# Performance work log

Hardware: AMD Instinct MI355X
Metric: run time of the kernel (lower is better)

Reference implementation:

```python
import jax, jax.numpy as jnp
import numpy as np

UP = 4  # FCUUp up_stride
EPS_FCU = 1e-6
EPS_NL = 1e-5


def setup_inputs() -> dict:
    key = jax.random.key(0)
    ks = jax.random.split(key, 24)
    B, E, C, CI = 8, 768, 256, 128
    H, W = 14, 14
    x_t = jax.random.normal(ks[0], (B, 1 + H * W, E), jnp.float32)
    x_cnn = jax.random.normal(ks[1], (B, C, H * UP, W * UP), jnp.float32)
    s = 0.02
    return {
        'x_t': x_t,
        'x_cnn': x_cnn,
        # FCUUp: conv_project (E->C) + BN
        'Wp': jax.random.normal(ks[2], (C, E), jnp.float32) * s,
        'bp': jnp.zeros((C,), jnp.float32),
        'g1': jnp.ones((C,), jnp.float32),
        'b1': jnp.zeros((C,), jnp.float32),
        'rm1': jax.random.normal(ks[3], (C,), jnp.float32) * 0.1,
        'rv1': jax.random.uniform(ks[4], (C,), jnp.float32, 0.5, 1.5),
        # NLBlockND (embedded): g, theta, phi 1x1 convs C->CI
        'Wg': jax.random.normal(ks[5], (CI, C), jnp.float32) * s,
        'bg': jnp.zeros((CI,), jnp.float32),
        'Wth': jax.random.normal(ks[6], (CI, C), jnp.float32) * s,
        'bth': jnp.zeros((CI,), jnp.float32),
        'Wph': jax.random.normal(ks[7], (CI, C), jnp.float32) * s,
        'bph': jnp.zeros((CI,), jnp.float32),
        # W_z: 1x1 conv CI->C + BN
        'Wz': jax.random.normal(ks[8], (C, CI), jnp.float32) * s,
        'bz': jnp.zeros((C,), jnp.float32),
        'g2': jax.random.normal(ks[9], (C,), jnp.float32) * 0.1,
        'b2': jax.random.normal(ks[10], (C,), jnp.float32) * 0.1,
        'rm2': jax.random.normal(ks[11], (C,), jnp.float32) * 0.1,
        'rv2': jax.random.uniform(ks[12], (C,), jnp.float32, 0.5, 1.5),
    }


def _bn(x, gamma, beta, mean, var, eps):
    # eval-mode BatchNorm2d over channel axis 1 of BCHW
    inv = gamma / jnp.sqrt(var + eps)
    return x * inv[None, :, None, None] + (beta - mean * inv)[None, :, None, None]


def _conv1x1(x, w, b):
    # x: BCHW, w: [O, C] -> BOHW
    return jnp.einsum('oc,bchw->bohw', w, x) + b[None, :, None, None]


def reference(x_t, x_cnn, Wp, bp, g1, b1, rm1, rv1, Wg, bg, Wth, bth, Wph, bph, Wz, bz, g2, b2, rm2, rv2):
    B, Nc, H2, W2 = x_cnn.shape
    H, W = H2 // UP, W2 // UP
    CI = Wg.shape[0]
    # --- FCUUp: tokens -> feature map ---
    xr = x_t[:, 1:].transpose(0, 2, 1).reshape(B, -1, H, W)  # B,E,H,W
    xr = jax.nn.relu(_bn(_conv1x1(xr, Wp, bp), g1, b1, rm1, rv1, EPS_FCU))
    x_up = jnp.repeat(jnp.repeat(xr, UP, axis=2), UP, axis=3)  # nearest interp -> B,C,H2,W2
    # --- NLBlockND embedded: this=x_cnn, other=x_up ---
    N = H2 * W2
    g_x = _conv1x1(x_cnn, Wg, bg).reshape(B, CI, N).transpose(0, 2, 1)   # B,N,CI
    theta = _conv1x1(x_cnn, Wth, bth).reshape(B, CI, N)                  # B,CI,N
    phi = _conv1x1(x_up, Wph, bph).reshape(B, CI, N)                     # B,CI,N
    f = jnp.einsum('bim,bin->bmn', phi, theta)  # B,N,N
    f_div_C = jax.nn.softmax(f, axis=-1)
    y = jnp.einsum('bmn,bni->bmi', f_div_C, g_x)          # B,N,CI
    y = y.transpose(0, 2, 1).reshape(B, CI, H2, W2)
    W_y = _bn(_conv1x1(y, Wz, bz), g2, b2, rm2, rv2, EPS_NL)
    return W_y + x_cnn
```

## Files before the change

kernel.cpp:

```cpp
#include <hip/hip_runtime.h>
#include <hip/hip_bf16.h>

#define B_ 8
#define E_ 768
#define C_ 256
#define CI_ 128
#define NQ_ 196
#define N_ 3136

typedef short bf16x8 __attribute__((ext_vector_type(8)));
typedef float f32x4 __attribute__((ext_vector_type(4)));

__device__ __forceinline__ ushort f2bf(float x) {
    union { float f; uint u; } v; v.f = x;
    uint r = v.u + 0x7FFFu + ((v.u >> 16) & 1u);
    return (ushort)(r >> 16);
}
__device__ __forceinline__ uint pack2(float a, float b) {
    return (uint)f2bf(a) | ((uint)f2bf(b) << 16);
}

__global__ __launch_bounds__(256) void k01(
    const float* __restrict__ x_cnn, ushort* __restrict__ xT,
    const float* __restrict__ Wth, const float* __restrict__ Wg,
    const float* __restrict__ Wph, const float* __restrict__ Wz,
    const float* __restrict__ x_t, const float* __restrict__ Wp,
    const float* __restrict__ bp, const float* __restrict__ g1, const float* __restrict__ b1,
    const float* __restrict__ rm1, const float* __restrict__ rv1,
    ushort* __restrict__ Wcomb, ushort* __restrict__ Wph_bf, ushort* __restrict__ Wz_bf,
    float* __restrict__ y_ws, float* __restrict__ rowsum, ushort* __restrict__ xact)
{
    __shared__ float Xs[64][68];
    __shared__ ushort Al[32 * 40];
    __shared__ ushort Bl[64 * 40];
    int bx = blockIdx.x;
    int t = threadIdx.x;

    if (bx >= 1824) {
        int bx2 = bx - 1824;
        int b = bx2 & 7; int rest = bx2 >> 3;
        int mt = rest & 7, nt = rest >> 3;
        int q0 = mt * 32, c0 = nt * 64;
        int lane = t & 63, w = t >> 6;

        int arow = t >> 3, ac4 = t & 7;
        bool arow_ok = (q0 + arow) < NQ_;
        const float* gax = x_t + (size_t)b * 197 * 768 + (size_t)(1 + q0 + arow) * 768 + ac4 * 4;
        int brow = t >> 2, bc = t & 3;
        const float* gbf = Wp + (size_t)(c0 + brow) * 768 + bc * 8;
        float binv = g1[c0 + brow] * rsqrtf(rv1[c0 + brow] + 1e-6f);
        ushort* la = &Al[arow * 40 + ac4 * 4];
        ushort* lb = &Bl[brow * 40 + bc * 8];

        f32x4 acc0 = (f32x4){0.f, 0.f, 0.f, 0.f};
        f32x4 acc1 = (f32x4){0.f, 0.f, 0.f, 0.f};
        int am = (lane & 15) * 40 + (lane >> 4) * 8;
        int bn = (w * 16 + (lane & 15)) * 40 + (lane >> 4) * 8;

        uint2 aw; aw.x = 0; aw.y = 0;
        if (arow_ok) { float4 x0 = *(const float4*)(gax); aw.x = pack2(x0.x, x0.y); aw.y = pack2(x0.z, x0.w); }
        uint4 bw;
        {
            float4 u = *(const float4*)(gbf), v = *(const float4*)(gbf + 4);
            bw.x = pack2(u.x * binv, u.y * binv); bw.y = pack2(u.z * binv, u.w * binv);
            bw.z = pack2(v.x * binv, v.y * binv); bw.w = pack2(v.z * binv, v.w * binv);
        }

        for (int ks = 0; ks < 24; ++ks) {
            __syncthreads();
            *(uint2*)la = aw;
            *(uint4*)lb = bw;
            __syncthreads();
            if (ks + 1 < 24) {
                aw.x = 0; aw.y = 0;
                if (arow_ok) {
                    float4 x0 = *(const float4*)(gax + (ks + 1) * 32);
                    aw.x = pack2(x0.x, x0.y); aw.y = pack2(x0.z, x0.w);
                }
                float4 u = *(const float4*)(gbf + (ks + 1) * 32);
                float4 v = *(const float4*)(gbf + (ks + 1) * 32 + 4);
                bw.x = pack2(u.x * binv, u.y * binv); bw.y = pack2(u.z * binv, u.w * binv);
                bw.z = pack2(v.x * binv, v.y * binv); bw.w = pack2(v.z * binv, v.w * binv);
            }
            bf16x8 af0 = *(const bf16x8*)(&Al[am]);
            bf16x8 af1 = *(const bf16x8*)(&Al[am + 16 * 40]);
            bf16x8 bfv = *(const bf16x8*)(&Bl[bn]);
            acc0 = __builtin_amdgcn_mfma_f32_16x16x32_bf16(af0, bfv, acc0, 0, 0, 0);
            acc1 = __builtin_amdgcn_mfma_f32_16x16x32_bf16(af1, bfv, acc1, 0, 0, 0);
        }

        int r4 = (lane >> 4) * 4;
        int cn = lane & 15;
        int c = c0 + w * 16 + cn;
        float inv1 = g1[c] * rsqrtf(rv1[c] + 1e-6f);
        float badd = bp[c] * inv1 + b1[c] - rm1[c] * inv1;
        #pragma unroll
        for (int r = 0; r < 4; ++r) {
            float v0 = fmaxf(acc0[r] + badd, 0.0f);
            float v1 = fmaxf(acc1[r] + badd, 0.0f);
            xact[((size_t)((b << 8) + q0 + r4 + r)) * 256 + c] = f2bf(v0);
            xact[((size_t)((b << 8) + q0 + 16 + r4 + r)) * 256 + c] = f2bf(v1);
        }
        return;
    }
    if (bx >= 1568) {
        int idx = (bx - 1568) * 256 + t;
        int o = idx >> 8, c = idx & 255;
        float v = (o < 128) ? Wth[o * 256 + c] : Wg[(o - 128) * 256 + c];
        Wcomb[idx] = f2bf(v);
        if (idx < 32768) Wph_bf[idx] = f2bf(Wph[idx]);
        if (idx < 32768) Wz_bf[idx] = f2bf(Wz[idx]);
        if (idx < 2048) rowsum[idx] = 0.0f;
        for (int i = idx; i < B_ * NQ_ * CI_; i += 65536) y_ws[i] = 0.0f;
        return;
    }
    int b = bx & 7; int rest = bx >> 3;
    int ct = rest & 3, nt = rest >> 2;
    int c0 = ct * 64, n0 = nt * 64;
    #pragma unroll
    for (int rr = 0; rr < 4; ++rr) {
        int idx = t + rr * 256;
        int c = idx >> 4, n4 = idx & 15;
        float4 v = *(const float4*)(x_cnn + ((size_t)(b * C_) + c0 + c) * N_ + n0 + n4 * 4);
        *(float4*)(&Xs[c][n4 * 4]) = v;
    }
    __syncthreads();
    int n = t & 63, cc = t >> 6;
    ushort vals[16];
    #pragma unroll
    for (int j = 0; j < 16; ++j)
        vals[j] = f2bf(Xs[cc * 16 + j][n]);
    ushort* outp = xT + ((size_t)(b * N_) + n0 + n) * 256 + c0 + cc * 16;
    *(uint4*)(outp) = *(const uint4*)(&vals[0]);
    *(uint4*)(outp + 8) = *(const uint4*)(&vals[8]);
}

__global__ __launch_bounds__(256) void k12(
    const ushort* __restrict__ Wcomb, const float* __restrict__ bth, const float* __restrict__ bg,
    const ushort* __restrict__ xT, ushort* __restrict__ thT, ushort* __restrict__ gT,
    const ushort* __restrict__ xact, const ushort* __restrict__ Wph_bf,
    const float* __restrict__ bph, ushort* __restrict__ phi_bf)
{
    __shared__ ushort Al[128 * 40];
    __shared__ ushort Bl[64 * 40];
    int t = threadIdx.x;
    int lane = t & 63, w = t >> 6;

    if (blockIdx.x >= 784) {
        int bx2 = blockIdx.x - 784;
        int b = bx2 & 7; int rest = bx2 >> 3;
        int mt = rest & 3, nt = rest >> 2;
        int q0 = mt * 64, i0 = nt * 64;
        int wm = w >> 1, wn = w & 1;
        int row = t >> 2, chunk = t & 3;

        const ushort* ga = xact + ((size_t)((b << 8) + q0 + row)) * 256 + chunk * 8;
        const ushort* gb = Wph_bf + (size_t)(i0 + row) * 256 + chunk * 8;
        ushort* la = &Al[row * 40 + chunk * 8];
        ushort* lb = &Bl[row * 40 + chunk * 8];

        f32x4 acc[2][2];
        #pragma unroll
        for (int a = 0; a < 2; ++a)
            #pragma unroll
            for (int bb = 0; bb < 2; ++bb) acc[a][bb] = (f32x4){0.f, 0.f, 0.f, 0.f};

        int am = (wm * 32 + (lane & 15)) * 40 + (lane >> 4) * 8;
        int bn = (wn * 32 + (lane & 15)) * 40 + (lane >> 4) * 8;

        uint4 aw = *(const uint4*)(ga);
        uint4 bw = *(const uint4*)(gb);
        for (int ks = 0; ks < 8; ++ks) {
            __syncthreads();
            *(uint4*)la = aw;
            *(uint4*)lb = bw;
            __syncthreads();
            if (ks + 1 < 8) {
                aw = *(const uint4*)(ga + (ks + 1) * 32);
                bw = *(const uint4*)(gb + (ks + 1) * 32);
            }
            bf16x8 af[2], bfv[2];
            #pragma unroll
            for (int fm = 0; fm < 2; ++fm) af[fm] = *(const bf16x8*)(&Al[am + fm * 16 * 40]);
            #pragma unroll
            for (int fn = 0; fn < 2; ++fn) bfv[fn] = *(const bf16x8*)(&Bl[bn + fn * 16 * 40]);
            #pragma unroll
            for (int fm = 0; fm < 2; ++fm)
                #pragma unroll
                for (int fn = 0; fn < 2; ++fn)
                    acc[fm][fn] = __builtin_amdgcn_mfma_f32_16x16x32_bf16(af[fm], bfv[fn], acc[fm][fn], 0, 0, 0);
        }

        int r4 = (lane >> 4) * 4;
        int cn = lane & 15;
        #pragma unroll
        for (int fn = 0; fn < 2; ++fn) {
            int i = i0 + wn * 32 + fn * 16 + cn;
            float bias = bph[i];
            #pragma unroll
            for (int fm = 0; fm < 2; ++fm) {
                int q = q0 + wm * 32 + fm * 16 + r4;
                #pragma unroll
                for (int r = 0; r < 4; ++r) {
                    ushort val = ((q + r) < NQ_) ? f2bf(acc[fm][fn][r] + bias) : (ushort)0;
                    phi_bf[((size_t)((b << 8) + q + r)) * 128 + i] = val;
                }
            }
        }
        return;
    }

    int bx = blockIdx.x;
    int b = bx & 7; int rest = bx >> 3;
    int mt = rest & 1, nt = rest >> 1;
    int o0 = mt * 128, n0 = nt * 64;
    int wm = w >> 1, wn = w & 1;
    int cn = lane & 15, kc = lane >> 4;

    int arow = t >> 1, ach = t & 1;
    const ushort* ga = Wcomb + (size_t)(o0 + arow) * 256 + ach * 8;
    int brow = t >> 2, bch = t & 3;
    const ushort* gb = xT + ((size_t)(b * N_) + n0 + brow) * 256 + bch * 8;
    ushort* la = &Al[arow * 40 + ach * 8];
    ushort* lb = &Bl[brow * 40 + bch * 8];

    f32x4 acc[4][2];
    #pragma unroll
    for (int a = 0; a < 4; ++a)
        #pragma unroll
        for (int bb = 0; bb < 2; ++bb) acc[a][bb] = (f32x4){0.f, 0.f, 0.f, 0.f};

    int am = (wm * 64 + cn) * 40 + kc * 8;
    int bn = (wn * 32 + cn) * 40 + kc * 8;

    uint4 aw0 = *(const uint4*)(ga);
    uint4 aw1 = *(const uint4*)(ga + 16);
    uint4 bw = *(const uint4*)(gb);
    for (int ks = 0; ks < 8; ++ks) {
        __syncthreads();
        *(uint4*)la = aw0;
        *(uint4*)(la + 16) = aw1;
        *(uint4*)lb = bw;
        __syncthreads();
        if (ks + 1 < 8) {
            aw0 = *(const uint4*)(ga + (ks + 1) * 32);
            aw1 = *(const uint4*)(ga + (ks + 1) * 32 + 16);
            bw = *(const uint4*)(gb + (ks + 1) * 32);
        }
        bf16x8 af[4], bfv[2];
        #pragma unroll
        for (int fm = 0; fm < 4; ++fm) af[fm] = *(const bf16x8*)(&Al[am + fm * 16 * 40]);
        #pragma unroll
        for (int fn = 0; fn < 2; ++fn) bfv[fn] = *(const bf16x8*)(&Bl[bn + fn * 16 * 40]);
        #pragma unroll
        for (int fm = 0; fm < 4; ++fm)
            #pragma unroll
            for (int fn = 0; fn < 2; ++fn)
                acc[fm][fn] = __builtin_amdgcn_mfma_f32_16x16x32_bf16(af[fm], bfv[fn], acc[fm][fn], 0, 0, 0);
    }

    int r4 = kc * 4;
    if (mt == 0) {
        #pragma unroll
        for (int fm = 0; fm < 4; ++fm) {
            int ob = wm * 64 + fm * 16 + r4;
            #pragma unroll
            for (int fn = 0; fn < 2; ++fn) {
                int n = n0 + wn * 32 + fn * 16 + cn;
                ushort4 v;
                v.x = f2bf(acc[fm][fn][0] + bth[ob + 0]);
                v.y = f2bf(acc[fm][fn][1] + bth[ob + 1]);
                v.z = f2bf(acc[fm][fn][2] + bth[ob + 2]);
                v.w = f2bf(acc[fm][fn][3] + bth[ob + 3]);
                *(ushort4*)(&thT[((size_t)(b * N_) + n) * 128 + ob]) = v;
            }
        }
    } else {
        #pragma unroll
        for (int fm = 0; fm < 4; ++fm) {
            int og = wm * 64 + fm * 16 + r4;
            #pragma unroll
            for (int fn = 0; fn < 2; ++fn) {
                int n = n0 + wn * 32 + fn * 16 + cn;
                #pragma unroll
                for (int r = 0; r < 4; ++r)
                    gT[((size_t)(b * 128) + og + r) * N_ + n] = f2bf(acc[fm][fn][r] + bg[og + r]);
            }
        }
    }
}

__global__ __launch_bounds__(256, 2) void k3_flash(
    const ushort* __restrict__ phi_bf, const ushort* __restrict__ thT,
    const ushort* __restrict__ gT, float* __restrict__ y_ws, float* __restrict__ rowsum)
{
    __shared__ ushort Qs[32 * 136];
    __shared__ ushort Kt[64 * 136];
    __shared__ ushort Gt[128 * 72];
    __shared__ ushort Ps[32 * 72];
    int bx = blockIdx.x;
    int b = bx & 7; int rr_ = bx >> 3;
    int qt = rr_ % 7, ksp = rr_ / 7;
    int q0 = qt * 32;
    int nb0 = ksp * 448;
    int t = threadIdx.x;
    int lane = t & 63, w = t >> 6;
    int cn = lane & 15, kc = lane >> 4;

    #pragma unroll
    for (int rr = 0; rr < 2; ++rr) {
        int idx = t + rr * 256;
        int q = idx >> 4, ch = idx & 15;
        uint4 v = *(const uint4*)(phi_bf + ((size_t)((b << 8) + q0 + q)) * 128 + ch * 8);
        *(uint4*)(&Qs[q * 136 + ch * 8]) = v;
    }

    int krow = t >> 2, kch = t & 3;
    int grow = t >> 1, gch = t & 1;
    const ushort* gK = thT + ((size_t)(b * N_) + nb0 + krow) * 128 + kch * 8;
    const ushort* gG = gT + ((size_t)(b * 128) + grow) * N_ + nb0 + gch * 8;
    ushort* lK = &Kt[krow * 136 + kch * 8];
    ushort* lG = &Gt[grow * 72 + gch * 8];

    float rs[2][4] = {{0, 0, 0, 0}, {0, 0, 0, 0}};
    f32x4 yacc[2][2];
    #pragma unroll
    for (int a = 0; a < 2; ++a)
        #pragma unroll
        for (int bb = 0; bb < 2; ++bb) yacc[a][bb] = (f32x4){0.f, 0.f, 0.f, 0.f};

    for (int s = 0; s < 7; ++s) {
        __syncthreads();
        {
            uint4 kv[4], gv[4];
            #pragma unroll
            for (int it = 0; it < 4; ++it) {
                kv[it] = *(const uint4*)(gK + it * 32);
                gv[it] = *(const uint4*)(gG + it * 16);
            }
            #pragma unroll
            for (int it = 0; it < 4; ++it) {
                *(uint4*)(lK + it * 32) = kv[it];
                *(uint4*)(lG + it * 16) = gv[it];
            }
        }
        gK += (size_t)64 * 128;
        gG += 64;
        __syncthreads();
        f32x4 f0 = (f32x4){0.f, 0.f, 0.f, 0.f};
        f32x4 f1 = (f32x4){0.f, 0.f, 0.f, 0.f};
        #pragma unroll
        for (int k4 = 0; k4 < 4; ++k4) {
            bf16x8 af0 = *(const bf16x8*)(&Qs[cn * 136 + k4 * 32 + kc * 8]);
            bf16x8 af1 = *(const bf16x8*)(&Qs[(16 + cn) * 136 + k4 * 32 + kc * 8]);
            bf16x8 bk = *(const bf16x8*)(&Kt[(w * 16 + cn) * 136 + k4 * 32 + kc * 8]);
            f0 = __builtin_amdgcn_mfma_f32_16x16x32_bf16(af0, bk, f0, 0, 0, 0);
            f1 = __builtin_amdgcn_mfma_f32_16x16x32_bf16(af1, bk, f1, 0, 0, 0);
        }
        #pragma unroll
        for (int r2 = 0; r2 < 4; ++r2) {
            float e0 = __expf(f0[r2]);
            float e1 = __expf(f1[r2]);
            rs[0][r2] += e0; rs[1][r2] += e1;
            Ps[(kc * 4 + r2) * 72 + w * 16 + cn] = f2bf(e0);
            Ps[(16 + kc * 4 + r2) * 72 + w * 16 + cn] = f2bf(e1);
        }
        __syncthreads();
        #pragma unroll
        for (int k2 = 0; k2 < 2; ++k2) {
            bf16x8 pa0 = *(const bf16x8*)(&Ps[cn * 72 + k2 * 32 + kc * 8]);
            bf16x8 pa1 = *(const bf16x8*)(&Ps[(16 + cn) * 72 + k2 * 32 + kc * 8]);
            bf16x8 g0 = *(const bf16x8*)(&Gt[(w * 32 + cn) * 72 + k2 * 32 + kc * 8]);
            bf16x8 g1 = *(const bf16x8*)(&Gt[(w * 32 + 16 + cn) * 72 + k2 * 32 + kc * 8]);
            yacc[0][0] = __builtin_amdgcn_mfma_f32_16x16x32_bf16(pa0, g0, yacc[0][0], 0, 0, 0);
            yacc[0][1] = __builtin_amdgcn_mfma_f32_16x16x32_bf16(pa0, g1, yacc[0][1], 0, 0, 0);
            yacc[1][0] = __builtin_amdgcn_mfma_f32_16x16x32_bf16(pa1, g0, yacc[1][0], 0, 0, 0);
            yacc[1][1] = __builtin_amdgcn_mfma_f32_16x16x32_bf16(pa1, g1, yacc[1][1], 0, 0, 0);
        }
    }

    #pragma unroll
    for (int fm = 0; fm < 2; ++fm) {
        #pragma unroll
        for (int fn = 0; fn < 2; ++fn) {
            int i = w * 32 + fn * 16 + cn;
            #pragma unroll
            for (int r2 = 0; r2 < 4; ++r2) {
                int q = q0 + fm * 16 + kc * 4 + r2;
                if (q < NQ_)
                    atomicAdd(&y_ws[((size_t)(b * NQ_) + q) * 128 + i], yacc[fm][fn][r2]);
            }
        }
    }
    #pragma unroll
    for (int off = 1; off <= 8; off <<= 1) {
        #pragma unroll
        for (int fm = 0; fm < 2; ++fm)
            #pragma unroll
            for (int r2 = 0; r2 < 4; ++r2)
                rs[fm][r2] += __shfl_xor(rs[fm][r2], off);
    }
    if (cn == 0) {
        #pragma unroll
        for (int fm = 0; fm < 2; ++fm)
            #pragma unroll
            for (int r2 = 0; r2 < 4; ++r2)
                atomicAdd(&rowsum[(b << 8) + q0 + fm * 16 + kc * 4 + r2], rs[fm][r2]);
    }
}

__global__ __launch_bounds__(256) void k45(
    const float* __restrict__ y_ws, const float* __restrict__ rowsum,
    const ushort* __restrict__ Wz_bf,
    const float* __restrict__ bz, const float* __restrict__ g2, const float* __restrict__ b2,
    const float* __restrict__ rm2, const float* __restrict__ rv2,
    const float* __restrict__ x_cnn, float* __restrict__ out)
{
    __shared__ ushort Al[16 * 136];
    __shared__ ushort Bl[256 * 40];
    __shared__ float zs[16 * 260];
    int bx = blockIdx.x;
    int b = bx & 7, hq = bx >> 3;
    int q0 = hq * 14;
    int t = threadIdx.x;
    int lane = t & 63, w = t >> 6;
    int cn = lane & 15, kc = lane >> 4;

    {
        int row = t >> 4, i0 = (t & 15) * 8;
        uint4 aw = make_uint4(0, 0, 0, 0);
        if (row < 14) {
            float inv = 1.0f / rowsum[(b << 8) + q0 + row];
            const float* yp = y_ws + ((size_t)(b * NQ_) + q0 + row) * 128 + i0;
            float4 u = *(const float4*)(yp), v = *(const float4*)(yp + 4);
            aw.x = pack2(u.x * inv, u.y * inv); aw.y = pack2(u.z * inv, u.w * inv);
            aw.z = pack2(v.x * inv, v.y * inv); aw.w = pack2(v.z * inv, v.w * inv);
        }
        *(uint4*)(&Al[row * 136 + i0]) = aw;
    }

    f32x4 acc[4];
    #pragma unroll
    for (int a = 0; a < 4; ++a) acc[a] = (f32x4){0.f, 0.f, 0.f, 0.f};
    int am = cn * 136 + kc * 8;
    int bn = (w * 64 + cn) * 40 + kc * 8;

    #pragma unroll
    for (int ks = 0; ks < 4; ++ks) {
        __syncthreads();
        {
            const ushort* wp = Wz_bf + (size_t)t * 128 + ks * 32;
            uint4 b0 = *(const uint4*)(wp);
            uint4 b1v = *(const uint4*)(wp + 8);
            *(uint4*)(&Bl[t * 40]) = b0;
            *(uint4*)(&Bl[t * 40 + 8]) = b1v;
        }
        __syncthreads();
        bf16x8 af = *(const bf16x8*)(&Al[am + ks * 32]);
        #pragma unroll
        for (int fc = 0; fc < 4; ++fc) {
            bf16x8 bv = *(const bf16x8*)(&Bl[bn + fc * 16 * 40]);
            acc[fc] = __builtin_amdgcn_mfma_f32_16x16x32_bf16(af, bv, acc[fc], 0, 0, 0);
        }
    }

    #pragma unroll
    for (int fc = 0; fc < 4; ++fc) {
        int c = w * 64 + fc * 16 + cn;
        float inv2 = g2[c] * rsqrtf(rv2[c] + 1e-5f);
        float add2 = b2[c] - rm2[c] * inv2;
        float bzc = bz[c];
        #pragma unroll
        for (int r = 0; r < 4; ++r) {
            int q = kc * 4 + r;
            zs[q * 260 + c] = (acc[fc][r] + bzc) * inv2 + add2;
        }
    }
    __syncthreads();

    if (t < 224) {
        int c4 = t / 14, w4 = t % 14;
        #pragma unroll
        for (int ccg = 0; ccg < 16; ++ccg) {
            int c = c4 * 16 + ccg;
            float z = zs[w4 * 260 + c];
            #pragma unroll
            for (int dh = 0; dh < 4; ++dh) {
                size_t off = ((size_t)(b * C_ + c)) * N_ + (size_t)(hq * 4 + dh) * 56 + w4 * 4;
                float4 xv = *(const float4*)(x_cnn + off);
                *(float4*)(out + off) = make_float4(xv.x + z, xv.y + z, xv.z + z, xv.w + z);
            }
        }
    }
}

extern "C" void kernel_launch(void* const* d_in, const int* in_sizes, int n_in,
                              void* d_out, int out_size, void* d_ws, size_t ws_size,
                              hipStream_t stream) {
    const float* x_t   = (const float*)d_in[0];
    const float* x_cnn = (const float*)d_in[1];
    const float* Wp  = (const float*)d_in[2];
    const float* bp  = (const float*)d_in[3];
    const float* g1  = (const float*)d_in[4];
    const float* b1  = (const float*)d_in[5];
    const float* rm1 = (const float*)d_in[6];
    const float* rv1 = (const float*)d_in[7];
    const float* Wg  = (const float*)d_in[8];
    const float* bg  = (const float*)d_in[9];
    const float* Wth = (const float*)d_in[10];
    const float* bth = (const float*)d_in[11];
    const float* Wph = (const float*)d_in[12];
    const float* bph = (const float*)d_in[13];
    const float* Wz  = (const float*)d_in[14];
    const float* bz  = (const float*)d_in[15];
    const float* g2  = (const float*)d_in[16];
    const float* b2  = (const float*)d_in[17];
    const float* rm2 = (const float*)d_in[18];
    const float* rv2 = (const float*)d_in[19];
    float* out = (float*)d_out;

    char* ws = (char*)d_ws;
    ushort* xT    = (ushort*)(ws);
    ushort* thT   = (ushort*)(ws + 12845056);
    ushort* gT    = (ushort*)(ws + 19267584);
    ushort* phi   = (ushort*)(ws + 25690112);
    float*  y_ws  = (float*)(ws + 26214400);
    ushort* Wcomb = (ushort*)(ws + 27017216);
    ushort* Wph_bf= (ushort*)(ws + 27148288);
    ushort* Wz_bf = (ushort*)(ws + 27213824);
    ushort* xact  = (ushort*)(ws + 27279360);
    float*  rowsum= (float*)(ws + 28327936);

    k01<<<dim3(2080), dim3(256), 0, stream>>>(x_cnn, xT, Wth, Wg, Wph, Wz, x_t, Wp,
                                              bp, g1, b1, rm1, rv1,
                                              Wcomb, Wph_bf, Wz_bf, y_ws, rowsum, xact);
    k12<<<dim3(848), dim3(256), 0, stream>>>(Wcomb, bth, bg, xT, thT, gT,
                                             xact, Wph_bf, bph, phi);
    k3_flash<<<dim3(392), dim3(256), 0, stream>>>(phi, thT, gT, y_ws, rowsum);
    k45<<<dim3(112), dim3(256), 0, stream>>>(y_ws, rowsum, Wz_bf, bz, g2, b2, rm2, rv2,
                                             x_cnn, out);
}
```

Before: 71.38 us.

## Halve key tile and split flash kernel across twice as many blocks

The attention kernel now processes 32-key tiles instead of 64 and splits the key range into 14 chunks of 224, doubling the grid to 784 blocks. Warps are remapped into a 2x2 layout over query halves and key/channel halves, so each MFMA stage does less work per wave. Occupancy hint rises to 3 blocks per SM to fill the GPU better. The cost is twice as many atomic adds into y_ws and rowsum, plus more barriers per unit of work.

Result: slower. 75.51 us (+5.8%).

```diff
diff --git a/kernel.cpp b/kernel.cpp
--- a/kernel.cpp
+++ b/kernel.cpp
@@ -290,122 +290,103 @@
     }
 }
 
-__global__ __launch_bounds__(256, 2) void k3_flash(
+__global__ __launch_bounds__(256, 3) void k3_flash(
     const ushort* __restrict__ phi_bf, const ushort* __restrict__ thT,
     const ushort* __restrict__ gT, float* __restrict__ y_ws, float* __restrict__ rowsum)
 {
     __shared__ ushort Qs[32 * 136];
-    __shared__ ushort Kt[64 * 136];
-    __shared__ ushort Gt[128 * 72];
-    __shared__ ushort Ps[32 * 72];
+    __shared__ ushort Kt[32 * 136];
+    __shared__ ushort Gt[128 * 40];
+    __shared__ ushort Ps[32 * 40];
     int bx = blockIdx.x;
     int b = bx & 7; int rr_ = bx >> 3;
     int qt = rr_ % 7, ksp = rr_ / 7;
     int q0 = qt * 32;
-    int nb0 = ksp * 448;
+    int nb0 = ksp * 224;
     int t = threadIdx.x;
     int lane = t & 63, w = t >> 6;
     int cn = lane & 15, kc = lane >> 4;
-
-    #pragma unroll
-    for (int rr = 0; rr < 2; ++rr) {
-        int idx = t + rr * 256;
+    int qh = w >> 1, nh = w & 1, ih = nh * 64;
+
+    #pragma unroll
+    for (int rr2 = 0; rr2 < 2; ++rr2) {
+        int idx = t + rr2 * 256;
         int q = idx >> 4, ch = idx & 15;
         uint4 v = *(const uint4*)(phi_bf + ((size_t)((b << 8) + q0 + q)) * 128 + ch * 8);
         *(uint4*)(&Qs[q * 136 + ch * 8]) = v;
     }
 
-    int krow = t >> 2, kch = t & 3;
+    int krow = t >> 3, kch = t & 7;
     int grow = t >> 1, gch = t & 1;
     const ushort* gK = thT + ((size_t)(b * N_) + nb0 + krow) * 128 + kch * 8;
     const ushort* gG = gT + ((size_t)(b * 128) + grow) * N_ + nb0 + gch * 8;
     ushort* lK = &Kt[krow * 136 + kch * 8];
-    ushort* lG = &Gt[grow * 72 + gch * 8];
-
-    float rs[2][4] = {{0, 0, 0, 0}, {0, 0, 0, 0}};
-    f32x4 yacc[2][2];
-    #pragma unroll
-    for (int a = 0; a < 2; ++a)
-        #pragma unroll
-        for (int bb = 0; bb < 2; ++bb) yacc[a][bb] = (f32x4){0.f, 0.f, 0.f, 0.f};
+    ushort* lG = &Gt[grow * 40 + gch * 8];
+
+    float rs[4] = {0, 0, 0, 0};
+    f32x4 yacc[4];
+    #pragma unroll
+    for (int a = 0; a < 4; ++a) yacc[a] = (f32x4){0.f, 0.f, 0.f, 0.f};
 
     for (int s = 0; s < 7; ++s) {
         __syncthreads();
         {
-            uint4 kv[4], gv[4];
-            #pragma unroll
-            for (int it = 0; it < 4; ++it) {
-                kv[it] = *(const uint4*)(gK + it * 32);
-                gv[it] = *(const uint4*)(gG + it * 16);
-            }
-            #pragma unroll
-            for (int it = 0; it < 4; ++it) {
-                *(uint4*)(lK + it * 32) = kv[it];
-                *(uint4*)(lG + it * 16) = gv[it];
-            }
-        }
-        gK += (size_t)64 * 128;
-        gG += 64;
+            uint4 k0v = *(const uint4*)(gK);
+            uint4 k1v = *(const uint4*)(gK + 64);
+            uint4 g0v = *(const uint4*)(gG);
+            uint4 g1v = *(const uint4*)(gG + 16);
+            *(uint4*)(lK) = k0v;
+            *(uint4*)(lK + 64) = k1v;
+            *(uint4*)(lG) = g0v;
+            *(uint4*)(lG + 16) = g1v;
+        }
+        gK += 32 * 128;
+        gG += 32;
         __syncthreads();
         f32x4 f0 = (f32x4){0.f, 0.f, 0.f, 0.f};
-        f32x4 f1 = (f32x4){0.f, 0.f, 0.f, 0.f};
         #pragma unroll
         for (int k4 = 0; k4 < 4; ++k4) {
-            bf16x8 af0 = *(const bf16x8*)(&Qs[cn * 136 + k4 * 32 + kc * 8]);
-            bf16x8 af1 = *(const bf16x8*)(&Qs[(16 + cn) * 136 + k4 * 32 + kc * 8]);
-            bf16x8 bk = *(const bf16x8*)(&Kt[(w * 16 + cn) * 136 + k4 * 32 + kc * 8]);
-            f0 = __builtin_amdgcn_mfma_f32_16x16x32_bf16(af0, bk, f0, 0, 0, 0);
-            f1 = __builtin_amdgcn_mfma_f32_16x16x32_bf16(af1, bk, f1, 0, 0, 0);
+            bf16x8 af = *(const bf16x8*)(&Qs[(qh * 16 + cn) * 136 + k4 * 32 + kc * 8]);
+            bf16x8 bk = *(const bf16x8*)(&Kt[(nh * 16 + cn) * 136 + k4 * 32 + kc * 8]);
+            f0 = __builtin_amdgcn_mfma_f32_16x16x32_bf16(af, bk, f0, 0, 0, 0);
         }
         #pragma unroll
         for (int r2 = 0; r2 < 4; ++r2) {
-            float e0 = __expf(f0[r2]);
-            float e1 = __expf(f1[r2]);
-            rs[0][r2] += e0; rs[1][r2] += e1;
-            Ps[(kc * 4 + r2) * 72 + w * 16 + cn] = f2bf(e0);
-            Ps[(16 + kc * 4 + r2) * 72 + w * 16 + cn] = f2bf(e1);
-        }
-        __syncthreads();
-        #pragma unroll
-        for (int k2 = 0; k2 < 2; ++k2) {
-            bf16x8 pa0 = *(const bf16x8*)(&Ps[cn * 72 + k2 * 32 + kc * 8]);
-            bf16x8 pa1 = *(const bf16x8*)(&Ps[(16 + cn) * 72 + k2 * 32 + kc * 8]);
-            bf16x8 g0 = *(const bf16x8*)(&Gt[(w * 32 + cn) * 72 + k2 * 32 + kc * 8]);
-            bf16x8 g1 = *(const bf16x8*)(&Gt[(w * 32 + 16 + cn) * 72 + k2 * 32 + kc * 8]);
-            yacc[0][0] = __builtin_amdgcn_mfma_f32_16x16x32_bf16(pa0, g0, yacc[0][0], 0, 0, 0);
-            yacc[0][1] = __builtin_amdgcn_mfma_f32_16x16x32_bf16(pa0, g1, yacc[0][1], 0, 0, 0);
-            yacc[1][0] = __builtin_amdgcn_mfma_f32_16x16x32_bf16(pa1, g0, yacc[1][0], 0, 0, 0);
-            yacc[1][1] = __builtin_amdgcn_mfma_f32_16x16x32_bf16(pa1, g1, yacc[1][1], 0, 0, 0);
-        }
-    }
-
-    #pragma unroll
-    for (int fm = 0; fm < 2; ++fm) {
-        #pragma unroll
-        for (int fn = 0; fn < 2; ++fn) {
-            int i = w * 32 + fn * 16 + cn;
-            #pragma unroll
-            for (int r2 = 0; r2 < 4; ++r2) {
-                int q = q0 + fm * 16 + kc * 4 + r2;
-                if (q < NQ_)
-                    atomicAdd(&y_ws[((size_t)(b * NQ_) + q) * 128 + i], yacc[fm][fn][r2]);
-            }
+            float e = __expf(f0[r2]);
+            rs[r2] += e;
+            Ps[(qh * 16 + kc * 4 + r2) * 40 + nh * 16 + cn] = f2bf(e);
+        }
+        __syncthreads();
+        bf16x8 pa = *(const bf16x8*)(&Ps[(qh * 16 + cn) * 40 + kc * 8]);
+        #pragma unroll
+        for (int fc = 0; fc < 4; ++fc) {
+            bf16x8 gv = *(const bf16x8*)(&Gt[(ih + fc * 16 + cn) * 40 + kc * 8]);
+            yacc[fc] = __builtin_amdgcn_mfma_f32_16x16x32_bf16(pa, gv, yacc[fc], 0, 0, 0);
+        }
+    }
+
+    #pragma unroll
+    for (int fc = 0; fc < 4; ++fc) {
+        int i = ih + fc * 16 + cn;
+        #pragma unroll
+        for (int r2 = 0; r2 < 4; ++r2) {
+            int q = q0 + qh * 16 + kc * 4 + r2;
+            if (q < NQ_)
+                atomicAdd(&y_ws[((size_t)(b * NQ_) + q) * 128 + i], yacc[fc][r2]);
         }
     }
     #pragma unroll
     for (int off = 1; off <= 8; off <<= 1) {
         #pragma unroll
-        for (int fm = 0; fm < 2; ++fm)
-            #pragma unroll
-            for (int r2 = 0; r2 < 4; ++r2)
-                rs[fm][r2] += __shfl_xor(rs[fm][r2], off);
+        for (int r2 = 0; r2 < 4; ++r2)
+            rs[r2] += __shfl_xor(rs[r2], off);
     }
     if (cn == 0) {
         #pragma unroll
-        for (int fm = 0; fm < 2; ++fm)
-            #pragma unroll
-            for (int r2 = 0; r2 < 4; ++r2)
-                atomicAdd(&rowsum[(b << 8) + q0 + fm * 16 + kc * 4 + r2], rs[fm][r2]);
+        for (int r2 = 0; r2 < 4; ++r2) {
+            int q = q0 + qh * 16 + kc * 4 + r2;
+            atomicAdd(&rowsum[(b << 8) + q], rs[r2]);
+        }
     }
 }
 
@@ -536,7 +517,7 @@
                                               Wcomb, Wph_bf, Wz_bf, y_ws, rowsum, xact);
     k12<<<dim3(848), dim3(256), 0, stream>>>(Wcomb, bth, bg, xT, thT, gT,
                                              xact, Wph_bf, bph, phi);
-    k3_flash<<<dim3(392), dim3(256), 0, stream>>>(phi, thT, gT, y_ws, rowsum);
+    k3_flash<<<dim3(784), dim3(256), 0, stream>>>(phi, thT, gT, y_ws, rowsum);
     k45<<<dim3(112), dim3(256), 0, stream>>>(y_ws, rowsum, Wz_bf, bz, g2, b2, rm2, rv2,
                                              x_cnn, out);
 }
```
